# Kernel tuning notes

Measured on AMD Instinct MI355X. Metric: run time of the kernel, lower is better.

## Reference

```python
import jax, jax.numpy as jnp
import numpy as np

N_NODES = 50000
N_EDGES = 300000
NODE_DIM = 128
HIDDEN = 256
BN_EPS = 1e-5
ROLL_SHIFT = 16


def setup_inputs() -> dict:
    key = jax.random.key(0)
    ks = jax.random.split(key, 8)
    node_feat = jax.random.normal(ks[0], (N_NODES, NODE_DIM), dtype=jnp.float32)
    edge_index = jax.random.randint(ks[1], (2, N_EDGES), 0, N_NODES, dtype=jnp.int64)
    W1 = jax.random.normal(ks[2], (2 * NODE_DIM, HIDDEN), dtype=jnp.float32) * 0.05
    b1 = jnp.zeros((HIDDEN,), dtype=jnp.float32)
    bn_gamma = jnp.ones((HIDDEN,), dtype=jnp.float32)
    bn_beta = jnp.zeros((HIDDEN,), dtype=jnp.float32)
    bn_mean = jax.random.normal(ks[3], (HIDDEN,), dtype=jnp.float32) * 0.1
    bn_var = jax.random.uniform(ks[4], (HIDDEN,), dtype=jnp.float32, minval=0.5, maxval=1.5)
    W2 = jax.random.normal(ks[5], (HIDDEN, 1), dtype=jnp.float32) * 0.05
    b2 = jnp.zeros((1,), dtype=jnp.float32)
    return {
        "node_feat": node_feat, "edge_index": edge_index,
        "W1": W1, "b1": b1,
        "bn_gamma": bn_gamma, "bn_beta": bn_beta,
        "bn_mean": bn_mean, "bn_var": bn_var,
        "W2": W2, "b2": b2,
    }


def reference(node_feat, edge_index, W1, b1, bn_gamma, bn_beta, bn_mean, bn_var, W2, b2):
    row, col = edge_index[0], edge_index[1]
    # [E, 2*node_dim]: gather endpoint features and concat
    edge_feat = jnp.concatenate([node_feat[row], node_feat[col]], axis=1)

    def mlp(x):
        h = x @ W1 + b1                                   # [E, H]
        # BatchNorm1d (eval mode: running stats)
        h = (h - bn_mean) * jax.lax.rsqrt(bn_var + BN_EPS) * bn_gamma + bn_beta
        h = jax.nn.relu(h)
        return (h @ W2 + b2).reshape(-1)                  # [E]

    edge_pred_1 = mlp(edge_feat)
    edge_pred_2 = mlp(jnp.roll(edge_feat, ROLL_SHIFT, axis=1))
    return jax.nn.sigmoid((edge_pred_1 + edge_pred_2) * 0.5)
```

## Files before the change

kernel.cpp:

```cpp
#include <hip/hip_runtime.h>
#include <hip/hip_bf16.h>

#define E_TOTAL 300000
#define N_NODES 50000
#define NDIM    128
#define KDIM    256
#define HDIM    512
#define BN_EPS  1e-5f
#define NTILES  ((E_TOTAL + 63) / 64)
#define NBLK    256
#define NF_BLOCKS 6250
#define LT_MAX  19
#define A_SCALE 24.0f

typedef __attribute__((ext_vector_type(4))) int   i32x4;
typedef __attribute__((ext_vector_type(4))) float f32x4;
typedef const __attribute__((address_space(1))) unsigned int* gas1_t;
typedef __attribute__((address_space(3))) unsigned int* las3_t;

__device__ __forceinline__ int q8(float x, float s) {
  float v = fminf(fmaxf(x * s, -127.f), 127.f);
  return (int)rintf(v);
}

#define DPP_STAGE(C)                                                          \
  {                                                                           \
    _Pragma("unroll")                                                         \
    for (int i = 0; i < 16; i++) {                                            \
      int t = __builtin_amdgcn_update_dpp(0, __float_as_int(vs[i]),           \
                                          (C), 0xF, 0xF, true);               \
      vs[i] += __int_as_float(t);                                             \
    }                                                                         \
  }

__global__ void prep_kernel(const float* __restrict__ nf, unsigned char* __restrict__ nfq,
                            const float* __restrict__ W1, const float* __restrict__ b1,
                            const float* __restrict__ gamma, const float* __restrict__ beta,
                            const float* __restrict__ mean, const float* __restrict__ var,
                            const float* __restrict__ W2,
                            unsigned char* __restrict__ Wswz,
                            float* __restrict__ cbias, float* __restrict__ w2c,
                            float* __restrict__ rinv) {
  int b = blockIdx.x;
  int tid = threadIdx.x;
  if (b < NF_BLOCKS) {
    int i = b * 256 + tid;
    float4 v = ((const float4*)nf)[i];
    int q0 = q8(v.x, A_SCALE), q1 = q8(v.y, A_SCALE);
    int q2 = q8(v.z, A_SCALE), q3 = q8(v.w, A_SCALE);
    ((unsigned*)nfq)[i] = (q0 & 255) | ((q1 & 255) << 8) | ((q2 & 255) << 16) | ((q3 & 255) << 24);
  } else if (b < NF_BLOCKS + 32) {
    int ct = b - NF_BLOCKS;
    __shared__ float amx[16][16];
    __shared__ float sB[16];
    {
      int cl = tid >> 4, pt = tid & 15;
      int jj = (ct * 16 + cl) & 255;
      float m = 0.f;
      #pragma unroll
      for (int i = 0; i < 16; i++)
        m = fmaxf(m, fabsf(W1[(pt * 16 + i) * 256 + jj]));
      amx[cl][pt] = m;
    }
    __syncthreads();
    if (tid < 16) {
      int jj = (ct * 16 + tid) & 255;
      float s = gamma[jj] * rsqrtf(var[jj] + BN_EPS);
      float m = 0.f;
      #pragma unroll
      for (int p = 0; p < 16; p++) m = fmaxf(m, amx[tid][p]);
      float amax_b = fmaxf(m * fabsf(s), 1e-20f);
      sB[tid] = 127.f / amax_b;
      rinv[ct * 16 + tid] = amax_b / (127.f * A_SCALE);
    }
    __syncthreads();
    {
      int kt   = tid >> 6;
      int lane = tid & 63;
      int l16  = lane & 15, quad = lane >> 4;
      int col  = ct * 16 + l16;
      int jj   = col & 255;
      int shift = (col >= 256) ? 16 : 0;
      float s  = gamma[jj] * rsqrtf(var[jj] + BN_EPS);
      float sc = sB[l16];
      unsigned o[4];
      #pragma unroll
      for (int d = 0; d < 4; d++) {
        unsigned pk = 0;
        #pragma unroll
        for (int jb = 0; jb < 4; jb++) {
          int k  = kt * 64 + quad * 16 + d * 4 + jb;
          int ks = (k + shift) & 255;
          int q  = q8(W1[ks * 256 + jj] * s, sc);
          pk |= (unsigned)(q & 255) << (8 * jb);
        }
        o[d] = pk;
      }
      *(uint4*)(Wswz + ((size_t)(ct * 4 + kt) * 64 + lane) * 16) = *(const uint4*)o;
    }
  } else {
    for (int j = tid; j < HDIM; j += 256) {
      int jj = j & 255;
      float s = gamma[jj] * rsqrtf(var[jj] + BN_EPS);
      cbias[j] = b1[jj] * s + beta[jj] - mean[jj] * s;
      w2c[j]  = 0.5f * W2[jj];
    }
  }
}

__global__ __launch_bounds__(512, 2) void edge_mlp_kernel(
    const unsigned char* __restrict__ nfq, const int* __restrict__ eidx,
    const unsigned char* __restrict__ Wswz, const float* __restrict__ cbias,
    const float* __restrict__ w2c, const float* __restrict__ rinv,
    const float* __restrict__ b2, float* __restrict__ out) {
  __shared__ unsigned char Ab[4][16 * 1024];
  __shared__ int idxl[LT_MAX * 128];
  __shared__ float partial[4][8][64];

  const int tid  = threadIdx.x;
  const int w    = tid >> 6;
  const int lane = tid & 63;
  const int l16  = lane & 15;
  const int quad = lane >> 4;
  const int b    = blockIdx.x;
  const int ntl  = (NTILES - b + NBLK - 1) / NBLK;

  const i32x4* Wf = (const i32x4*)Wswz;
  i32x4 bq[4][4];
  #pragma unroll
  for (int n = 0; n < 4; n++)
    #pragma unroll
    for (int kt = 0; kt < 4; kt++)
      bq[n][kt] = Wf[((w * 4 + n) * 4 + kt) * 64 + lane];

  float cj[4], w2j[4], rv[4];
  #pragma unroll
  for (int n = 0; n < 4; n++) {
    int j = w * 64 + n * 16 + l16;
    cj[n]  = cbias[j];
    w2j[n] = w2c[j];
    rv[n]  = rinv[j];
  }
  const float b2v = b2[0];

  for (int g = tid; g < ntl * 128; g += 512) {
    int lt2 = g >> 7, r = g & 127;
    int half = r >> 6;
    int e = (b + lt2 * NBLK) * 64 + (r & 63);
    if (e >= E_TOTAL) e = E_TOTAL - 1;
    idxl[g] = eidx[half * E_TOTAL + e];
  }
  __syncthreads();

  const int smt   = w >> 1;
  const int shalf = w & 1;
  const int sfrag0 = smt * 4 + shalf * 2;

  auto stage = [&](int lt2, int slot) {
    int node = idxl[lt2 * 128 + shalf * 64 + smt * 16 + l16];
    const unsigned char* gbase = nfq + (size_t)node * NDIM + quad * 16;
    #pragma unroll
    for (int i = 0; i < 2; i++)
      __builtin_amdgcn_global_load_lds((gas1_t)(gbase + i * 64),
                                       (las3_t)(&Ab[slot][(sfrag0 + i) * 1024]),
                                       16, 0, 0);
  };

  auto combine = [&](int lt2, int le) {
    int e = (b + lt2 * NBLK) * 64 + le;
    if (e < E_TOTAL) {
      float s = 0.f;
      #pragma unroll
      for (int ww = 0; ww < 8; ww++) s += partial[lt2 & 3][ww][le];
      out[e] = 1.0f / (1.0f + __expf(-(s + b2v)));
    }
  };

  auto compute_tile = [&](int lt2) {
    i32x4 acc[4][4] = {};
    const unsigned char* Ap = &Ab[lt2 & 3][lane * 16];
    #pragma unroll
    for (int kt = 0; kt < 4; kt++) {
      i32x4 af[4];
      #pragma unroll
      for (int mt = 0; mt < 4; mt++)
        af[mt] = *(const i32x4*)(Ap + (mt * 4 + kt) * 1024);
      #pragma unroll
      for (int n = 0; n < 4; n++)
        #pragma unroll
        for (int mt = 0; mt < 4; mt++)
          acc[mt][n] = __builtin_amdgcn_mfma_i32_16x16x64_i8(af[mt], bq[n][kt], acc[mt][n], 0, 0, 0);
    }

    float vs[16];
    #pragma unroll
    for (int mt = 0; mt < 4; mt++)
      #pragma unroll
      for (int r = 0; r < 4; r++) {
        float v = 0.f;
        #pragma unroll
        for (int n = 0; n < 4; n++) {
          float h = (float)acc[mt][n][r] * rv[n] + cj[n];
          v += fmaxf(h, 0.f) * w2j[n];
        }
        vs[mt * 4 + r] = v;
      }
    DPP_STAGE(0x128)
    DPP_STAGE(0x124)
    DPP_STAGE(0x122)
    DPP_STAGE(0x121)
    if (l16 == 0) {
      #pragma unroll
      for (int mt = 0; mt < 4; mt++)
        #pragma unroll
        for (int r = 0; r < 4; r++)
          partial[lt2 & 3][w][mt * 16 + quad * 4 + r] = vs[mt * 4 + r];
    }
  };

  stage(0, 0);
  if (1 < ntl) stage(1, 1);

  for (int lt = 0; lt < ntl; lt += 2) {
    __syncthreads();

    int s2 = lt + 2, s3 = lt + 3;
    if (s2 < ntl) stage(s2, s2 & 3);
    if (s3 < ntl) stage(s3, s3 & 3);

    if (lt >= 2) {
      if (tid < 64)       combine(lt - 2, tid);
      else if (tid < 128) combine(lt - 1, tid - 64);
    }

    compute_tile(lt);
    if (lt + 1 < ntl) compute_tile(lt + 1);
  }

  __syncthreads();
  if ((ntl & 1) == 0) {
    if (tid < 64)       combine(ntl - 2, tid);
    else if (tid < 128) combine(ntl - 1, tid - 64);
  } else {
    if (tid < 64)       combine(ntl - 1, tid);
  }
}

extern "C" void kernel_launch(void* const* d_in, const int* in_sizes, int n_in,
                              void* d_out, int out_size, void* d_ws, size_t ws_size,
                              hipStream_t stream) {
  const float* node_feat = (const float*)d_in[0];
  const int*   eidx      = (const int*)d_in[1];
  const float* W1        = (const float*)d_in[2];
  const float* b1        = (const float*)d_in[3];
  const float* gamma     = (const float*)d_in[4];
  const float* beta      = (const float*)d_in[5];
  const float* mean      = (const float*)d_in[6];
  const float* var       = (const float*)d_in[7];
  const float* W2        = (const float*)d_in[8];
  const float* b2        = (const float*)d_in[9];
  float* out = (float*)d_out;

  unsigned char* Wswz = (unsigned char*)d_ws;
  float* cbias = (float*)((char*)d_ws + (size_t)HDIM * KDIM);
  float* w2c   = cbias + HDIM;
  float* rinv  = w2c + HDIM;
  unsigned char* nfq = (unsigned char*)(rinv + HDIM);

  prep_kernel<<<NF_BLOCKS + 33, 256, 0, stream>>>(node_feat, nfq, W1, b1, gamma, beta,
                                                  mean, var, W2, Wswz, cbias, w2c, rinv);

  edge_mlp_kernel<<<NBLK, 512, 0, stream>>>(nfq, eidx, Wswz, cbias, w2c, rinv, b2, out);
}
```

Baseline: 141.5 us.

## Swap MFMA operands so hidden dim is rows and fold dequant scale into bias/W2

The MFMA now takes the weights as the A operand and the gathered edge features as B, so each lane's accumulator rows index hidden units instead of edges. The per-column dequant scale is folded into a precomputed bias (cj/rv) and into W2 (w2*rv), which removes a multiply per element in the epilogue and turns it into an FMA chain. The reduction across hidden units becomes two cross-quad shuffles instead of four DPP stages over 16 values. The separate prep block for the bias and W2 constants is merged into the weight-quantization blocks. The cost is more per-lane constant registers (32 floats instead of 12).

```diff
diff --git a/kernel.cpp b/kernel.cpp
--- a/kernel.cpp
+++ b/kernel.cpp
@@ -14,7 +14,6 @@
 #define A_SCALE 24.0f
 
 typedef __attribute__((ext_vector_type(4))) int   i32x4;
-typedef __attribute__((ext_vector_type(4))) float f32x4;
 typedef const __attribute__((address_space(1))) unsigned int* gas1_t;
 typedef __attribute__((address_space(3))) unsigned int* las3_t;
 
@@ -22,16 +21,6 @@
   float v = fminf(fmaxf(x * s, -127.f), 127.f);
   return (int)rintf(v);
 }
-
-#define DPP_STAGE(C)                                                          \
-  {                                                                           \
-    _Pragma("unroll")                                                         \
-    for (int i = 0; i < 16; i++) {                                            \
-      int t = __builtin_amdgcn_update_dpp(0, __float_as_int(vs[i]),           \
-                                          (C), 0xF, 0xF, true);               \
-      vs[i] += __int_as_float(t);                                             \
-    }                                                                         \
-  }
 
 __global__ void prep_kernel(const float* __restrict__ nf, unsigned char* __restrict__ nfq,
                             const float* __restrict__ W1, const float* __restrict__ b1,
@@ -39,8 +28,7 @@
                             const float* __restrict__ mean, const float* __restrict__ var,
                             const float* __restrict__ W2,
                             unsigned char* __restrict__ Wswz,
-                            float* __restrict__ cbias, float* __restrict__ w2c,
-                            float* __restrict__ rinv) {
+                            float* __restrict__ cb2, float* __restrict__ wp2) {
   int b = blockIdx.x;
   int tid = threadIdx.x;
   if (b < NF_BLOCKS) {
@@ -49,7 +37,7 @@
     int q0 = q8(v.x, A_SCALE), q1 = q8(v.y, A_SCALE);
     int q2 = q8(v.z, A_SCALE), q3 = q8(v.w, A_SCALE);
     ((unsigned*)nfq)[i] = (q0 & 255) | ((q1 & 255) << 8) | ((q2 & 255) << 16) | ((q3 & 255) << 24);
-  } else if (b < NF_BLOCKS + 32) {
+  } else {
     int ct = b - NF_BLOCKS;
     __shared__ float amx[16][16];
     __shared__ float sB[16];
@@ -64,14 +52,18 @@
     }
     __syncthreads();
     if (tid < 16) {
-      int jj = (ct * 16 + tid) & 255;
+      int j  = ct * 16 + tid;
+      int jj = j & 255;
       float s = gamma[jj] * rsqrtf(var[jj] + BN_EPS);
       float m = 0.f;
       #pragma unroll
       for (int p = 0; p < 16; p++) m = fmaxf(m, amx[tid][p]);
       float amax_b = fmaxf(m * fabsf(s), 1e-20f);
       sB[tid] = 127.f / amax_b;
-      rinv[ct * 16 + tid] = amax_b / (127.f * A_SCALE);
+      float rv = amax_b / (127.f * A_SCALE);
+      float cj = b1[jj] * s + beta[jj] - mean[jj] * s;
+      cb2[j] = cj / rv;
+      wp2[j] = 0.5f * W2[jj] * rv;
     }
     __syncthreads();
     {
@@ -98,21 +90,14 @@
       }
       *(uint4*)(Wswz + ((size_t)(ct * 4 + kt) * 64 + lane) * 16) = *(const uint4*)o;
     }
-  } else {
-    for (int j = tid; j < HDIM; j += 256) {
-      int jj = j & 255;
-      float s = gamma[jj] * rsqrtf(var[jj] + BN_EPS);
-      cbias[j] = b1[jj] * s + beta[jj] - mean[jj] * s;
-      w2c[j]  = 0.5f * W2[jj];
-    }
   }
 }
 
 __global__ __launch_bounds__(512, 2) void edge_mlp_kernel(
     const unsigned char* __restrict__ nfq, const int* __restrict__ eidx,
-    const unsigned char* __restrict__ Wswz, const float* __restrict__ cbias,
-    const float* __restrict__ w2c, const float* __restrict__ rinv,
-    const float* __restrict__ b2, float* __restrict__ out) {
+    const unsigned char* __restrict__ Wswz, const float* __restrict__ cb2,
+    const float* __restrict__ wp2, const float* __restrict__ b2,
+    float* __restrict__ out) {
   __shared__ unsigned char Ab[4][16 * 1024];
   __shared__ int idxl[LT_MAX * 128];
   __shared__ float partial[4][8][64];
@@ -128,19 +113,20 @@
   const i32x4* Wf = (const i32x4*)Wswz;
   i32x4 bq[4][4];
   #pragma unroll
-  for (int n = 0; n < 4; n++)
+  for (int mt = 0; mt < 4; mt++)
     #pragma unroll
     for (int kt = 0; kt < 4; kt++)
-      bq[n][kt] = Wf[((w * 4 + n) * 4 + kt) * 64 + lane];
-
-  float cj[4], w2j[4], rv[4];
+      bq[mt][kt] = Wf[((w * 4 + mt) * 4 + kt) * 64 + lane];
+
+  float c2[16], wv[16];
   #pragma unroll
-  for (int n = 0; n < 4; n++) {
-    int j = w * 64 + n * 16 + l16;
-    cj[n]  = cbias[j];
-    w2j[n] = w2c[j];
-    rv[n]  = rinv[j];
-  }
+  for (int mt = 0; mt < 4; mt++)
+    #pragma unroll
+    for (int r = 0; r < 4; r++) {
+      int j = w * 64 + mt * 16 + quad * 4 + r;
+      c2[mt * 4 + r] = cb2[j];
+      wv[mt * 4 + r] = wp2[j];
+    }
   const float b2v = b2[0];
 
   for (int g = tid; g < ntl * 128; g += 512) {
@@ -152,12 +138,12 @@
   }
   __syncthreads();
 
-  const int smt   = w >> 1;
-  const int shalf = w & 1;
-  const int sfrag0 = smt * 4 + shalf * 2;
+  const int snt   = w & 3;
+  const int shalf = w >> 2;
+  const int sfrag0 = snt * 4 + shalf * 2;
 
   auto stage = [&](int lt2, int slot) {
-    int node = idxl[lt2 * 128 + shalf * 64 + smt * 16 + l16];
+    int node = idxl[lt2 * 128 + shalf * 64 + snt * 16 + l16];
     const unsigned char* gbase = nfq + (size_t)node * NDIM + quad * 16;
     #pragma unroll
     for (int i = 0; i < 2; i++)
@@ -181,40 +167,38 @@
     const unsigned char* Ap = &Ab[lt2 & 3][lane * 16];
     #pragma unroll
     for (int kt = 0; kt < 4; kt++) {
-      i32x4 af[4];
-      #pragma unroll
-      for (int mt = 0; mt < 4; mt++)
-        af[mt] = *(const i32x4*)(Ap + (mt * 4 + kt) * 1024);
-      #pragma unroll
-      for (int n = 0; n < 4; n++)
+      i32x4 ef[4];
+      #pragma unroll
+      for (int nt = 0; nt < 4; nt++)
+        ef[nt] = *(const i32x4*)(Ap + (nt * 4 + kt) * 1024);
+      #pragma unroll
+      for (int nt = 0; nt < 4; nt++)
         #pragma unroll
         for (int mt = 0; mt < 4; mt++)
-          acc[mt][n] = __builtin_amdgcn_mfma_i32_16x16x64_i8(af[mt], bq[n][kt], acc[mt][n], 0, 0, 0);
-    }
-
-    float vs[16];
-    #pragma unroll
-    for (int mt = 0; mt < 4; mt++)
-      #pragma unroll
-      for (int r = 0; r < 4; r++) {
-        float v = 0.f;
-        #pragma unroll
-        for (int n = 0; n < 4; n++) {
-          float h = (float)acc[mt][n][r] * rv[n] + cj[n];
-          v += fmaxf(h, 0.f) * w2j[n];
-        }
-        vs[mt * 4 + r] = v;
-      }
-    DPP_STAGE(0x128)
-    DPP_STAGE(0x124)
-    DPP_STAGE(0x122)
-    DPP_STAGE(0x121)
-    if (l16 == 0) {
+          acc[mt][nt] = __builtin_amdgcn_mfma_i32_16x16x64_i8(bq[mt][kt], ef[nt], acc[mt][nt], 0, 0, 0);
+    }
+
+    float vnt[4];
+    #pragma unroll
+    for (int nt = 0; nt < 4; nt++) {
+      float v = 0.f;
       #pragma unroll
       for (int mt = 0; mt < 4; mt++)
         #pragma unroll
-        for (int r = 0; r < 4; r++)
-          partial[lt2 & 3][w][mt * 16 + quad * 4 + r] = vs[mt * 4 + r];
+        for (int r = 0; r < 4; r++) {
+          float h = (float)acc[mt][nt][r] + c2[mt * 4 + r];
+          v = fmaf(fmaxf(h, 0.f), wv[mt * 4 + r], v);
+        }
+      vnt[nt] = v;
+    }
+    #pragma unroll
+    for (int nt = 0; nt < 4; nt++) vnt[nt] += __shfl_xor(vnt[nt], 16);
+    #pragma unroll
+    for (int nt = 0; nt < 4; nt++) vnt[nt] += __shfl_xor(vnt[nt], 32);
+    if (quad == 0) {
+      #pragma unroll
+      for (int nt = 0; nt < 4; nt++)
+        partial[lt2 & 3][w][nt * 16 + l16] = vnt[nt];
     }
   };
 
@@ -262,13 +246,12 @@
   float* out = (float*)d_out;
 
   unsigned char* Wswz = (unsigned char*)d_ws;
-  float* cbias = (float*)((char*)d_ws + (size_t)HDIM * KDIM);
-  float* w2c   = cbias + HDIM;
-  float* rinv  = w2c + HDIM;
-  unsigned char* nfq = (unsigned char*)(rinv + HDIM);
-
-  prep_kernel<<<NF_BLOCKS + 33, 256, 0, stream>>>(node_feat, nfq, W1, b1, gamma, beta,
-                                                  mean, var, W2, Wswz, cbias, w2c, rinv);
-
-  edge_mlp_kernel<<<NBLK, 512, 0, stream>>>(nfq, eidx, Wswz, cbias, w2c, rinv, b2, out);
-}
+  float* cb2 = (float*)((char*)d_ws + (size_t)HDIM * KDIM);
+  float* wp2 = cb2 + HDIM;
+  unsigned char* nfq = (unsigned char*)(wp2 + HDIM);
+
+  prep_kernel<<<NF_BLOCKS + 32, 256, 0, stream>>>(node_feat, nfq, W1, b1, gamma, beta,
+                                                  mean, var, W2, Wswz, cb2, wp2);
+
+  edge_mlp_kernel<<<NBLK, 512, 0, stream>>>(nfq, eidx, Wswz, cb2, wp2, b2, out);
+}
```

After: 136.7 us. -3.4%, faster.
